# Optimization experiments

Measured on AMD Instinct MI355X. Metric: run time of the kernel, lower is better.

## Reference

```python
import jax, jax.numpy as jnp
import numpy as np

B, ROI, DIN = 1024, 200, 200
ENDS = [41, 70, 91, 110, 130, 137, 158, 200]
STARTS = [0] + ENDS[:-1]
NSUB = len(ENDS)
SEG = np.concatenate([np.full(e - s, i) for i, (s, e) in enumerate(zip(STARTS, ENDS))])  # [ROI]
COUNTS = np.array(ENDS) - np.array(STARTS)
MEAN_MAT = np.zeros((NSUB, ROI), dtype=np.float32)
MEAN_MAT[SEG, np.arange(ROI)] = 1.0 / COUNTS[SEG]
EPS = 1e-5


def _leaky(x):
    return jax.nn.leaky_relu(x, 0.2)


def _bn2d(x, g, b):
    # torch BatchNorm1d (training): biased var over batch dim
    m = x.mean(0)
    v = x.var(0)
    return (x - m) * jax.lax.rsqrt(v + EPS) * g + b


def _bn3d(x, g, b):
    # x: [B, C, L]; stats over (B, L) per channel
    m = x.mean(axis=(0, 2), keepdims=True)
    v = x.var(axis=(0, 2), keepdims=True)
    return (x - m) * jax.lax.rsqrt(v + EPS) * g[None, :, None] + b[None, :, None]


def _block(x, rs_intra, rs_inter, mean_mat, seg):
    # einsum 'ijk,ijp->ijp' == row-sum scaling
    intra = rs_intra * x                                   # [B,R,F]
    sub = jnp.einsum('sr,brf->bsf', mean_mat, x)           # segment means [B,8,F]
    sub = rs_inter * sub                                   # inter row-sum scaling
    prop = sub[:, seg, :]                                  # broadcast back to nodes
    return (intra + prop) * 0.5


def setup_inputs() -> dict:
    key = jax.random.key(0)
    ks = jax.random.split(key, 24)
    s = 0.05
    d = {
        'adjacency_matrix': jax.random.uniform(ks[0], (B, ROI, ROI), jnp.float32),
        'intra_adjacency': jax.random.uniform(ks[1], (B, ROI, ROI), jnp.float32),
        'inter_adjacency': jax.random.uniform(ks[2], (B, NSUB, NSUB), jnp.float32),
        'node_features': jax.random.normal(ks[3], (B, ROI, DIN), jnp.float32),
        'W0': jax.random.normal(ks[4], (DIN, ROI)) * s, 'b0': jnp.zeros((ROI,)),
        'W1': jax.random.normal(ks[5], (ROI, ROI)) * s, 'b1': jnp.zeros((ROI,)),
        'g1': jnp.ones((ROI,)), 'be1': jnp.zeros((ROI,)),
        'W2': jax.random.normal(ks[6], (ROI, ROI)) * s, 'b2': jnp.zeros((ROI,)),
        'g2': jnp.ones((ROI,)), 'be2': jnp.zeros((ROI,)),
        'W3': jax.random.normal(ks[7], (ROI, 64)) * s, 'b3': jnp.zeros((64,)),
        'W4': jax.random.normal(ks[8], (64, 8)) * s, 'b4': jnp.zeros((8,)),
        'g3': jnp.ones((ROI,)), 'be3': jnp.zeros((ROI,)),
        'Wc1': jax.random.normal(ks[9], (8 * ROI, 256)) * s, 'bc1': jnp.zeros((256,)),
        'Wc2': jax.random.normal(ks[10], (256, 32)) * s, 'bc2': jnp.zeros((32,)),
        'Wc3': jax.random.normal(ks[11], (32, 2)) * s, 'bc3': jnp.zeros((2,)),
    }
    return d


def reference(adjacency_matrix, intra_adjacency, inter_adjacency, node_features,
              W0, b0, W1, b1, g1, be1, W2, b2, g2, be2,
              W3, b3, W4, b4, g3, be3, Wc1, bc1, Wc2, bc2, Wc3, bc3):
    mean_mat = jnp.asarray(MEAN_MAT)
    seg = jnp.asarray(SEG)
    rs_intra = intra_adjacency.sum(-1, keepdims=True)   # [B,R,1]
    rs_inter = inter_adjacency.sum(-1, keepdims=True)   # [B,8,1]

    x = _block(node_features, rs_intra, rs_inter, mean_mat, seg)
    x = _leaky(x @ W0 + b0) @ W1 + b1                    # gcn -> [B,R,ROI]
    x = _bn2d(x.reshape(B * ROI, ROI), g1, be1).reshape(B, ROI, ROI)

    x = _block(x, rs_intra, rs_inter, mean_mat, seg)
    x = _leaky(x @ W2 + b2)                              # gcn1
    x = _bn2d(x.reshape(B * ROI, ROI), g2, be2).reshape(B, ROI, ROI)

    x = _block(x, rs_intra, rs_inter, mean_mat, seg)
    x = _leaky(_leaky(x @ W3 + b3) @ W4 + b4)            # gcn2 -> [B,R,8]
    x = _bn3d(x, g3, be3)

    x = x.reshape(B, 8 * ROI)
    x = _leaky(x @ Wc1 + bc1)
    x = _leaky(x @ Wc2 + bc2)
    return x @ Wc3 + bc3
```

## Files before the change

kernel.cpp:

```cpp
#include <hip/hip_runtime.h>
#include <hip/hip_bf16.h>

#define BDIM 1024
#define ROI 200
#define DIN 200
#define NSUB 8
#define NROWS (BDIM * ROI)
#define XELEMS ((size_t)NROWS * 200)
#define PLPAD 32
#define PLSZ (XELEMS + PLPAD)

typedef __attribute__((ext_vector_type(8))) short short8;
typedef __attribute__((ext_vector_type(4))) float f32x4;

__device__ __constant__ float d_invcnt[8] = {
    1.f/41.f, 1.f/29.f, 1.f/21.f, 1.f/19.f, 1.f/20.f, 1.f/7.f, 1.f/21.f, 1.f/42.f};

__device__ inline unsigned short f2bf_rn(float x) {
  unsigned u = __float_as_uint(x);
  return (unsigned short)((u + 0x7FFFu + ((u >> 16) & 1u)) >> 16);
}
__device__ constexpr int seg_of_c(int r) {
  return (r < 41) ? 0 : (r < 70) ? 1 : (r < 91) ? 2 : (r < 110) ? 3
       : (r < 130) ? 4 : (r < 137) ? 5 : (r < 158) ? 6 : 7;
}

__device__ inline void gload_lds16(const unsigned short* src, unsigned short* dst) {
  __builtin_amdgcn_global_load_lds(
      (const __attribute__((address_space(1))) void*)src,
      (__attribute__((address_space(3))) void*)dst, 16, 0, 0);
}

__device__ inline void aburst7(const unsigned short* pA, const unsigned short* pB,
                               short8 (&aA)[7], short8 (&aB)[7]) {
  #pragma unroll
  for (int i = 0; i < 7; ++i) {
    aA[i] = *(const short8*)(pA + i * 32);
    aB[i] = *(const short8*)(pB + i * 32);
  }
}

__global__ __launch_bounds__(256) void rowsum4_k(const float* __restrict__ in,
                                                 float* __restrict__ out) {
  int row = blockIdx.x * 4 + (threadIdx.x >> 6);
  int lane = threadIdx.x & 63;
  const float* p = in + (size_t)row * 200;
  float v = p[lane] + p[lane + 64] + p[lane + 128];
  if (lane < 8) v += p[lane + 192];
  #pragma unroll
  for (int off = 32; off > 0; off >>= 1) v += __shfl_down(v, off);
  if (lane == 0) out[row] = v;
}

__global__ __launch_bounds__(256) void intersum_k(const float* __restrict__ in,
                                                  float* __restrict__ out) {
  int i = blockIdx.x * blockDim.x + threadIdx.x;
  if (i >= BDIM * NSUB) return;
  const float* p = in + (size_t)i * 8;
  float v = 0.f;
  #pragma unroll
  for (int c = 0; c < 8; ++c) v += p[c];
  out[i] = v;
}

template<int INPL, int BN>
__global__ __launch_bounds__(128) void seg_combine_bf_k(
    const float* __restrict__ xf, const unsigned short* __restrict__ xp,
    const float* __restrict__ rsI, const float* __restrict__ rsP,
    const float* __restrict__ ss, unsigned short* __restrict__ yp) {
  int b = blockIdx.x;
  int t = threadIdx.x;
  if (t >= 100) return;
  int c0 = 2 * t;
  size_t base = (size_t)b * 40000 + c0;
  float sc0 = 1.f, sh0 = 0.f, sc1 = 1.f, sh1 = 0.f;
  if (BN) { sc0 = ss[c0]; sh0 = ss[200 + c0]; sc1 = ss[c0 + 1]; sh1 = ss[200 + c0 + 1]; }
  float a0[8] = {0,0,0,0,0,0,0,0};
  float a1[8] = {0,0,0,0,0,0,0,0};
  #pragma unroll
  for (int r = 0; r < 200; ++r) {
    size_t idx = base + (size_t)r * 200;
    float v0, v1;
    if (INPL) {
      unsigned u = *(const unsigned*)(xp + idx);
      v0 = __uint_as_float(u << 16);
      v1 = __uint_as_float(u & 0xFFFF0000u);
    } else {
      float2 fv = *(const float2*)(xf + idx);
      v0 = fv.x; v1 = fv.y;
    }
    int s = seg_of_c(r);
    a0[s] += v0; a1[s] += v1;
  }
  float pr0[8], pr1[8];
  #pragma unroll
  for (int s = 0; s < 8; ++s) {
    float m0 = a0[s] * d_invcnt[s];
    float m1 = a1[s] * d_invcnt[s];
    if (BN) { m0 = m0 * sc0 + sh0; m1 = m1 * sc1 + sh1; }
    float rp = rsP[b * 8 + s];
    pr0[s] = rp * m0; pr1[s] = rp * m1;
  }
  const float* rsIb = rsI + b * 200;
  #pragma unroll
  for (int r = 0; r < 200; ++r) {
    size_t idx = base + (size_t)r * 200;
    float v0, v1;
    if (INPL) {
      unsigned u = *(const unsigned*)(xp + idx);
      v0 = __uint_as_float(u << 16);
      v1 = __uint_as_float(u & 0xFFFF0000u);
    } else {
      float2 fv = *(const float2*)(xf + idx);
      v0 = fv.x; v1 = fv.y;
    }
    if (BN) { v0 = v0 * sc0 + sh0; v1 = v1 * sc1 + sh1; }
    int s = seg_of_c(r);
    float ri = rsIb[r];
    float y0 = 0.5f * (ri * v0 + pr0[s]);
    float y1 = 0.5f * (ri * v1 + pr1[s]);
    unsigned o = (unsigned)f2bf_rn(y0) | ((unsigned)f2bf_rn(y1) << 16);
    *(unsigned*)(yp + idx) = o;
  }
}

__global__ __launch_bounds__(256) void wconv3_k(const float* __restrict__ W, int K, int N,
                                                int NFRAG, int NB, int KSTEPS,
                                                unsigned short* __restrict__ dst) {
  int total = NB * KSTEPS * NFRAG * 64 * 8;
  int idx = blockIdx.x * 256 + threadIdx.x;
  if (idx >= total) return;
  int j = idx & 7;
  int lane = (idx >> 3) & 63;
  int rest = idx >> 9;
  int frag = rest % NFRAG;
  int rest2 = rest / NFRAG;
  int ks = rest2 % KSTEPS;
  int cb = rest2 / KSTEPS;
  int k = ks * 32 + ((lane >> 4) << 3) + j;
  int col = cb * NFRAG * 16 + frag * 16 + (lane & 15);
  float v = (k < K && col < N) ? W[(size_t)k * N + col] : 0.f;
  dst[idx] = f2bf_rn(v);
}

template<int ACT, int STATS>
__global__ __launch_bounds__(512, 1) void gemm_bf3_k(
    const unsigned short* __restrict__ A, const unsigned short* __restrict__ Wf,
    const float* __restrict__ bias, unsigned short* __restrict__ Cp,
    float* __restrict__ stats) {
  constexpr int G = 7 * 7 * 64;
  __shared__ unsigned short wlds[G * 8];
  __shared__ unsigned short abuf[8][2][400 * 8];
  __shared__ float s_sum[112];
  __shared__ float s_sq[112];
  int tid = threadIdx.x;
  int lane = tid & 63;
  int wid = tid >> 6;
  int cb = blockIdx.y;

  const unsigned short* wsrc = Wf + (size_t)cb * G * 8;
  for (int g0 = wid * 64; g0 < G; g0 += 512)
    gload_lds16(wsrc + (size_t)(g0 + lane) * 8, &wlds[(size_t)g0 * 8]);
  if (STATS && tid < 112) { s_sum[tid] = 0.f; s_sq[tid] = 0.f; }

  int gw = blockIdx.x * 8 + wid;
  const int stride = 1024, nt = 12800;
  int row = lane & 15;
  int laneg = lane >> 4;

  auto issue_tile = [&](int t, unsigned short* buf) {
    const unsigned short* src = A + (size_t)t * 3200;
    #pragma unroll
    for (int j = 0; j < 7; ++j) {
      int slot = j * 64 + lane;
      if (slot < 400)
        gload_lds16(src + (size_t)slot * 8, buf + (size_t)j * 512);
    }
  };

  issue_tile(gw, &abuf[wid][0][0]);
  issue_tile(gw + stride, &abuf[wid][1][0]);
  __syncthreads();

  float lsum[7], lsq[7];
  #pragma unroll
  for (int f = 0; f < 7; ++f) { lsum[f] = 0.f; lsq[f] = 0.f; }
  int colbase = cb * 112;

  for (int i = 0; ; ++i) {
    int t = gw + i * stride;
    if (t >= nt) break;
    if (i) {
      asm volatile("s_waitcnt vmcnt(35)" ::: "memory");
      __builtin_amdgcn_sched_barrier(0);
    }
    const unsigned short* ab = &abuf[wid][i & 1][0];
    f32x4 acc[7];
    #pragma unroll
    for (int f = 0; f < 7; ++f) acc[f] = 0.0f;
    #pragma unroll
    for (int ks = 0; ks < 7; ++ks) {
      int cs = ks * 4 + laneg;
      if (cs > 24) cs = 0;
      short8 av = *(const short8*)&ab[(size_t)(row * 25 + cs) * 8];
      const short8* wp = (const short8*)wlds + (size_t)(ks * 7) * 64 + lane;
      #pragma unroll
      for (int f = 0; f < 7; ++f) {
        short8 wv = wp[(size_t)f * 64];
        acc[f] = __builtin_amdgcn_mfma_f32_16x16x32_bf16(av, wv, acc[f], 0, 0, 0);
      }
    }
    asm volatile("s_waitcnt lgkmcnt(0)" ::: "memory");
    __builtin_amdgcn_sched_barrier(0);
    int row0 = t * 16 + laneg * 4;
    #pragma unroll
    for (int f = 0; f < 7; ++f) {
      int col = colbase + f * 16 + row;
      if (col < 200) {
        float b = bias[col];
        #pragma unroll
        for (int r = 0; r < 4; ++r) {
          float v = acc[f][r] + b;
          if (ACT) v = (v >= 0.f) ? v : 0.2f * v;
          Cp[(size_t)(row0 + r) * 200 + col] = f2bf_rn(v);
          if (STATS) { lsum[f] += v; lsq[f] += v * v; }
        }
      }
    }
    __builtin_amdgcn_sched_barrier(0);
    int t2 = t + 2 * stride;
    issue_tile(t2 < nt ? t2 : gw, &abuf[wid][i & 1][0]);
    __builtin_amdgcn_sched_barrier(0);
  }

  if (STATS) {
    #pragma unroll
    for (int f = 0; f < 7; ++f) {
      float s = lsum[f] + __shfl_xor(lsum[f], 16) ;
      s += __shfl_xor(s, 32);
      float q = lsq[f] + __shfl_xor(lsq[f], 16);
      q += __shfl_xor(q, 32);
      if (laneg == 0) {
        atomicAdd(&s_sum[f * 16 + row], s);
        atomicAdd(&s_sq[f * 16 + row], q);
      }
    }
    __syncthreads();
    if (tid < 112) {
      int col = colbase + tid;
      if (col < 200) {
        atomicAdd(&stats[col], s_sum[tid]);
        atomicAdd(&stats[200 + col], s_sq[tid]);
      }
    }
  }
}

__global__ __launch_bounds__(256, 2) void gemm_w34_k(
    const unsigned short* __restrict__ A, const unsigned short* __restrict__ W3f,
    const unsigned short* __restrict__ W4f, const float* __restrict__ b3,
    const float* __restrict__ b4, unsigned short* __restrict__ xcls) {
  __shared__ unsigned short w3lds[7 * 4 * 64 * 8];
  __shared__ unsigned short w4lds[2 * 64 * 8];
  __shared__ unsigned short h3buf[128][72];
  int tid = threadIdx.x;
  int lane = tid & 63;
  int wid = tid >> 6;

  for (int g0 = wid * 64; g0 < 1792; g0 += 256)
    gload_lds16(W3f + (size_t)(g0 + lane) * 8, &w3lds[(size_t)g0 * 8]);
  for (int g0 = wid * 64; g0 < 128; g0 += 256)
    gload_lds16(W4f + (size_t)(g0 + lane) * 8, &w4lds[(size_t)g0 * 8]);

  const unsigned short* baseA = A + (size_t)(lane & 15) * 200 + ((lane >> 4) << 3);
  int r0 = (lane >> 4) * 4;

  short8 aA0[7], aB0[7], aA1[7], aB1[7];
  {
    size_t off = (size_t)(blockIdx.x * 128 + wid * 32) * 200;
    aburst7(baseA + off, baseA + off + 16 * 200, aA0, aB0);
  }
  __builtin_amdgcn_sched_barrier(0);
  __syncthreads();

  #pragma unroll
  for (int t = 0; t < 4; ++t) {
    int rt = blockIdx.x + 400 * t;
    int row0 = rt * 128 + wid * 32;
    if (t < 3) {
      size_t off = (size_t)((rt + 400) * 128 + wid * 32) * 200;
      if (t & 1) aburst7(baseA + off, baseA + off + 16 * 200, aA0, aB0);
      else       aburst7(baseA + off, baseA + off + 16 * 200, aA1, aB1);
      __builtin_amdgcn_sched_barrier(0);
    }
    f32x4 accA[4], accB[4];
    #pragma unroll
    for (int f = 0; f < 4; ++f) { accA[f] = 0.0f; accB[f] = 0.0f; }
    #pragma unroll
    for (int ks = 0; ks < 7; ++ks) {
      const short8* wp = (const short8*)w3lds + (size_t)(ks * 4) * 64 + lane;
      short8 av = (t & 1) ? aA1[ks] : aA0[ks];
      short8 bv = (t & 1) ? aB1[ks] : aB0[ks];
      #pragma unroll
      for (int f = 0; f < 4; ++f) {
        short8 wv = wp[(size_t)f * 64];
        accA[f] = __builtin_amdgcn_mfma_f32_16x16x32_bf16(av, wv, accA[f], 0, 0, 0);
        accB[f] = __builtin_amdgcn_mfma_f32_16x16x32_bf16(bv, wv, accB[f], 0, 0, 0);
      }
    }
    #pragma unroll
    for (int f = 0; f < 4; ++f) {
      int col = f * 16 + (lane & 15);
      float bb = b3[col];
      #pragma unroll
      for (int r = 0; r < 4; ++r) {
        float v = accA[f][r] + bb;
        v = (v >= 0.f) ? v : 0.2f * v;
        h3buf[wid * 32 + r0 + r][col] = f2bf_rn(v);
        v = accB[f][r] + bb;
        v = (v >= 0.f) ? v : 0.2f * v;
        h3buf[wid * 32 + 16 + r0 + r][col] = f2bf_rn(v);
      }
    }
    f32x4 acc2A = 0.0f, acc2B = 0.0f;
    #pragma unroll
    for (int ks = 0; ks < 2; ++ks) {
      short8 a2A = *(const short8*)&h3buf[wid * 32 + (lane & 15)][ks * 32 + ((lane >> 4) << 3)];
      short8 a2B = *(const short8*)&h3buf[wid * 32 + 16 + (lane & 15)][ks * 32 + ((lane >> 4) << 3)];
      short8 wv = *(const short8*)&w4lds[(size_t)(ks * 64 + lane) * 8];
      acc2A = __builtin_amdgcn_mfma_f32_16x16x32_bf16(a2A, wv, acc2A, 0, 0, 0);
      acc2B = __builtin_amdgcn_mfma_f32_16x16x32_bf16(a2B, wv, acc2B, 0, 0, 0);
    }
    int col = lane & 15;
    if (col < 8) {
      float bb = b4[col];
      #pragma unroll
      for (int r = 0; r < 4; ++r) {
        int row = row0 + r0 + r;
        float v = acc2A[r] + bb;
        v = (v >= 0.f) ? v : 0.2f * v;
        xcls[(size_t)(row / 200) * 1600 + (row % 200) * 8 + col] = f2bf_rn(v);
        int row2 = row + 16;
        v = acc2B[r] + bb;
        v = (v >= 0.f) ? v : 0.2f * v;
        xcls[(size_t)(row2 / 200) * 1600 + (row2 % 200) * 8 + col] = f2bf_rn(v);
      }
    }
  }
}

__global__ __launch_bounds__(256) void bn_scale_k(const float* __restrict__ stats,
                                                  const float* __restrict__ g,
                                                  const float* __restrict__ be,
                                                  float invN,
                                                  float* __restrict__ ss) {
  int c = threadIdx.x;
  if (c >= 200) return;
  float m = stats[c] * invN;
  float var = stats[200 + c] * invN - m * m;
  float sc = rsqrtf(var + 1e-5f) * g[c];
  ss[c] = sc;
  ss[200 + c] = be[c] - m * sc;
}

__global__ __launch_bounds__(256) void bn3d_stats_bf_k(const unsigned short* __restrict__ x,
                                                       float* __restrict__ stats) {
  int t = threadIdx.x;
  if (t >= 200) return;
  const unsigned short* p = x + (size_t)blockIdx.x * 16 * 1600 + t * 8;
  float s = 0.f, q = 0.f;
  for (int b = 0; b < 16; ++b) {
    const unsigned* u = (const unsigned*)(p + (size_t)b * 1600);
    #pragma unroll
    for (int i = 0; i < 4; ++i) {
      unsigned w = u[i];
      float v0 = __uint_as_float(w << 16);
      float v1 = __uint_as_float(w & 0xFFFF0000u);
      s += v0 + v1;
      q += v0 * v0 + v1 * v1;
    }
  }
  atomicAdd(&stats[t], s);
  atomicAdd(&stats[200 + t], q);
}

__global__ __launch_bounds__(256) void wcls_conv_k(const float* __restrict__ Wc1,
                                                   const float* __restrict__ ss,
                                                   unsigned short* __restrict__ dst) {
  int idx = blockIdx.x * 256 + threadIdx.x;
  if (idx >= 409600) return;
  int j = idx & 7;
  int lane = (idx >> 3) & 63;
  int rest = idx >> 9;
  int frag = rest & 3;
  int rest2 = rest >> 2;
  int ks = rest2 % 10;
  int slice = rest2 / 10;
  int kc = slice % 5, cb = slice / 5;
  int k = kc * 320 + ks * 32 + ((lane >> 4) << 3) + j;
  int col = cb * 64 + frag * 16 + (lane & 15);
  dst[idx] = f2bf_rn(Wc1[(size_t)k * 256 + col] * ss[k >> 3]);
}

__global__ __launch_bounds__(256) void bias1_init_k(const float* __restrict__ bc1,
                                                    float* __restrict__ bias1p) {
  bias1p[threadIdx.x] = bc1[threadIdx.x];
}
__global__ __launch_bounds__(256) void bias1_acc_k(const float* __restrict__ Wc1,
                                                   const float* __restrict__ ss,
                                                   float* __restrict__ bias1p) {
  int t = threadIdx.x;
  int k0 = blockIdx.x * 100;
  float a = 0.f;
  #pragma unroll 4
  for (int k = k0; k < k0 + 100; ++k)
    a += ss[200 + (k >> 3)] * Wc1[(size_t)k * 256 + t];
  atomicAdd(&bias1p[t], a);
}

__global__ __launch_bounds__(256, 3) void gemm_cls1_k(
    const unsigned short* __restrict__ xcls, const unsigned short* __restrict__ Wf,
    float* __restrict__ h1f) {
  __shared__ unsigned short wlds[10 * 4 * 64 * 8];
  int tid = threadIdx.x;
  int lane = tid & 63;
  int wid = tid >> 6;
  const unsigned short* wsrc = Wf + (size_t)(blockIdx.y * 5 + blockIdx.z) * (10 * 4 * 64) * 8;
  for (int g0 = wid * 64; g0 < 2560; g0 += 256)
    gload_lds16(wsrc + (size_t)(g0 + lane) * 8, &wlds[(size_t)g0 * 8]);

  int row0 = blockIdx.x * 128 + wid * 32;
  int kbase = blockIdx.z * 320;
  const unsigned short* pA = xcls + (size_t)(row0 + (lane & 15)) * 1600 + kbase + ((lane >> 4) << 3);
  const unsigned short* pB = pA + 16 * 1600;
  short8 aA[10], aB[10];
  #pragma unroll
  for (int i = 0; i < 10; ++i) {
    aA[i] = *(const short8*)(pA + i * 32);
    aB[i] = *(const short8*)(pB + i * 32);
  }
  __builtin_amdgcn_sched_barrier(0);
  __syncthreads();

  f32x4 accA[4], accB[4];
  #pragma unroll
  for (int f = 0; f < 4; ++f) { accA[f] = 0.0f; accB[f] = 0.0f; }
  #pragma unroll
  for (int ks = 0; ks < 10; ++ks) {
    const short8* wp = (const short8*)wlds + (size_t)(ks * 4) * 64 + lane;
    #pragma unroll
    for (int f = 0; f < 4; ++f) {
      short8 wv = wp[(size_t)f * 64];
      accA[f] = __builtin_amdgcn_mfma_f32_16x16x32_bf16(aA[ks], wv, accA[f], 0, 0, 0);
      accB[f] = __builtin_amdgcn_mfma_f32_16x16x32_bf16(aB[ks], wv, accB[f], 0, 0, 0);
    }
  }
  int colbase = blockIdx.y * 64;
  int r0 = (lane >> 4) * 4;
  #pragma unroll
  for (int f = 0; f < 4; ++f) {
    int col = colbase + f * 16 + (lane & 15);
    #pragma unroll
    for (int r = 0; r < 4; ++r) {
      atomicAdd(&h1f[(size_t)(row0 + r0 + r) * 256 + col], accA[f][r]);
      atomicAdd(&h1f[(size_t)(row0 + 16 + r0 + r) * 256 + col], accB[f][r]);
    }
  }
}

__global__ __launch_bounds__(256) void classifier2_k(
    const float* __restrict__ h1f, const float* __restrict__ bias1p,
    const float* __restrict__ Wc2, const float* __restrict__ bc2,
    const float* __restrict__ Wc3, const float* __restrict__ bc3,
    float* __restrict__ out) {
  __shared__ float h1s[8][256];
  __shared__ float h2s[8][32];
  int t = threadIdx.x;
  int b0 = blockIdx.x * 8;
  #pragma unroll
  for (int j = 0; j < 8; ++j) {
    float v = h1f[(size_t)(b0 + j) * 256 + t] + bias1p[t];
    h1s[j][t] = (v >= 0.f) ? v : 0.2f * v;
  }
  __syncthreads();
  {
    int j = t >> 5, c = t & 31;
    float a = 0.f;
    #pragma unroll 8
    for (int k = 0; k < 256; ++k) a += h1s[j][k] * Wc2[k * 32 + c];
    float v = a + bc2[c];
    h2s[j][c] = (v >= 0.f) ? v : 0.2f * v;
  }
  __syncthreads();
  if (t < 16) {
    int j = t >> 1, c = t & 1;
    float a = 0.f;
    #pragma unroll
    for (int k = 0; k < 32; ++k) a += h2s[j][k] * Wc3[k * 2 + c];
    out[(size_t)(b0 + j) * 2 + c] = a + bc3[c];
  }
}

extern "C" void kernel_launch(void* const* d_in, const int* in_sizes, int n_in,
                              void* d_out, int out_size, void* d_ws, size_t ws_size,
                              hipStream_t stream) {
  const float* intra = (const float*)d_in[1];
  const float* inter = (const float*)d_in[2];
  const float* nodef = (const float*)d_in[3];
  const float* W0 = (const float*)d_in[4];
  const float* b0 = (const float*)d_in[5];
  const float* W1 = (const float*)d_in[6];
  const float* b1 = (const float*)d_in[7];
  const float* g1 = (const float*)d_in[8];
  const float* be1 = (const float*)d_in[9];
  const float* W2 = (const float*)d_in[10];
  const float* b2 = (const float*)d_in[11];
  const float* g2 = (const float*)d_in[12];
  const float* be2 = (const float*)d_in[13];
  const float* W3 = (const float*)d_in[14];
  const float* b3 = (const float*)d_in[15];
  const float* W4 = (const float*)d_in[16];
  const float* b4 = (const float*)d_in[17];
  const float* g3 = (const float*)d_in[18];
  const float* be3 = (const float*)d_in[19];
  const float* Wc1 = (const float*)d_in[20];
  const float* bc1 = (const float*)d_in[21];
  const float* Wc2 = (const float*)d_in[22];
  const float* bc2 = (const float*)d_in[23];
  const float* Wc3 = (const float*)d_in[24];
  const float* bc3 = (const float*)d_in[25];
  float* out = (float*)d_out;

  unsigned short* P0 = (unsigned short*)d_ws;
  unsigned short* P1 = P0 + PLSZ;
  float* fbase = (float*)(P1 + PLSZ);
  float* rsI  = fbase;
  float* rsP  = rsI + NROWS;
  float* stats = rsP + BDIM * 8;
  float* ssbuf = stats + 512;
  float* h1f  = ssbuf + 512;
  float* bias1p = h1f + (size_t)BDIM * 256;
  unsigned short* wt = (unsigned short*)(bias1p + 512);
  const size_t W200SZ = 2 * 7 * 7 * 64 * 8;
  const size_t W3SZ   = 1 * 7 * 4 * 64 * 8;
  const size_t W4SZ   = 1 * 2 * 1 * 64 * 8;
  unsigned short* w0f = wt;
  unsigned short* w1f = w0f + W200SZ;
  unsigned short* w2f = w1f + W200SZ;
  unsigned short* w3f = w2f + W200SZ;
  unsigned short* w4f = w3f + W3SZ;
  unsigned short* wc1f = w4f + W4SZ;
  unsigned short* xcls = P0;

  hipMemsetAsync(P0 + XELEMS, 0, PLPAD * 2, stream);
  hipMemsetAsync(P1 + XELEMS, 0, PLPAD * 2, stream);

  wconv3_k<<<(int)((W200SZ + 255) / 256), 256, 0, stream>>>(W0, 200, 200, 7, 2, 7, w0f);
  wconv3_k<<<(int)((W200SZ + 255) / 256), 256, 0, stream>>>(W1, 200, 200, 7, 2, 7, w1f);
  wconv3_k<<<(int)((W200SZ + 255) / 256), 256, 0, stream>>>(W2, 200, 200, 7, 2, 7, w2f);
  wconv3_k<<<(int)((W3SZ + 255) / 256), 256, 0, stream>>>(W3, 200, 64, 4, 1, 7, w3f);
  wconv3_k<<<(int)((W4SZ + 255) / 256), 256, 0, stream>>>(W4, 64, 8, 1, 1, 2, w4f);

  rowsum4_k<<<NROWS / 4, 256, 0, stream>>>(intra, rsI);
  intersum_k<<<(BDIM * 8 + 255) / 256, 256, 0, stream>>>(inter, rsP);

  seg_combine_bf_k<0, 0><<<BDIM, 128, 0, stream>>>(
      nodef, nullptr, rsI, rsP, nullptr, P0);

  gemm_bf3_k<1, 0><<<dim3(128, 2), 512, 0, stream>>>(P0, w0f, b0, P1, nullptr);
  hipMemsetAsync(stats, 0, 400 * sizeof(float), stream);
  gemm_bf3_k<0, 1><<<dim3(128, 2), 512, 0, stream>>>(P1, w1f, b1, P0, stats);
  bn_scale_k<<<1, 256, 0, stream>>>(stats, g1, be1, 1.f / (float)NROWS, ssbuf);

  seg_combine_bf_k<1, 1><<<BDIM, 128, 0, stream>>>(
      nullptr, P0, rsI, rsP, ssbuf, P1);

  hipMemsetAsync(stats, 0, 400 * sizeof(float), stream);
  gemm_bf3_k<1, 1><<<dim3(128, 2), 512, 0, stream>>>(P1, w2f, b2, P0, stats);
  bn_scale_k<<<1, 256, 0, stream>>>(stats, g2, be2, 1.f / (float)NROWS, ssbuf);

  seg_combine_bf_k<1, 1><<<BDIM, 128, 0, stream>>>(
      nullptr, P0, rsI, rsP, ssbuf, P1);

  gemm_w34_k<<<400, 256, 0, stream>>>(P1, w3f, w4f, b3, b4, xcls);

  hipMemsetAsync(stats, 0, 400 * sizeof(float), stream);
  bn3d_stats_bf_k<<<64, 256, 0, stream>>>(xcls, stats);
  bn_scale_k<<<1, 256, 0, stream>>>(stats, g3, be3, 1.f / 8192.f, ssbuf);

  wcls_conv_k<<<1600, 256, 0, stream>>>(Wc1, ssbuf, wc1f);
  bias1_init_k<<<1, 256, 0, stream>>>(bc1, bias1p);
  bias1_acc_k<<<16, 256, 0, stream>>>(Wc1, ssbuf, bias1p);

  hipMemsetAsync(h1f, 0, (size_t)BDIM * 256 * sizeof(float), stream);
  gemm_cls1_k<<<dim3(8, 4, 5), 256, 0, stream>>>(xcls, wc1f, h1f);
  classifier2_k<<<BDIM / 8, 256, 0, stream>>>(h1f, bias1p, Wc2, bc2, Wc3, bc3, out);
}
```

Before: 429.4 us.

## Rewrite W3/W4 GEMM as persistent kernel with async LDS double-buffering

```diff
diff --git a/kernel.cpp b/kernel.cpp
--- a/kernel.cpp
+++ b/kernel.cpp
@@ -29,15 +29,6 @@
   __builtin_amdgcn_global_load_lds(
       (const __attribute__((address_space(1))) void*)src,
       (__attribute__((address_space(3))) void*)dst, 16, 0, 0);
-}
-
-__device__ inline void aburst7(const unsigned short* pA, const unsigned short* pB,
-                               short8 (&aA)[7], short8 (&aB)[7]) {
-  #pragma unroll
-  for (int i = 0; i < 7; ++i) {
-    aA[i] = *(const short8*)(pA + i * 32);
-    aB[i] = *(const short8*)(pB + i * 32);
-  }
 }
 
 __global__ __launch_bounds__(256) void rowsum4_k(const float* __restrict__ in,
@@ -191,7 +182,7 @@
     int t = gw + i * stride;
     if (t >= nt) break;
     if (i) {
-      asm volatile("s_waitcnt vmcnt(35)" ::: "memory");
+      asm volatile("s_waitcnt vmcnt(24)" ::: "memory");
       __builtin_amdgcn_sched_barrier(0);
     }
     const unsigned short* ab = &abuf[wid][i & 1][0];
@@ -236,7 +227,7 @@
   if (STATS) {
     #pragma unroll
     for (int f = 0; f < 7; ++f) {
-      float s = lsum[f] + __shfl_xor(lsum[f], 16) ;
+      float s = lsum[f] + __shfl_xor(lsum[f], 16);
       s += __shfl_xor(s, 32);
       float q = lsq[f] + __shfl_xor(lsq[f], 16);
       q += __shfl_xor(q, 32);
@@ -256,96 +247,102 @@
   }
 }
 
-__global__ __launch_bounds__(256, 2) void gemm_w34_k(
+__global__ __launch_bounds__(512, 1) void gemm_w34s_k(
     const unsigned short* __restrict__ A, const unsigned short* __restrict__ W3f,
     const unsigned short* __restrict__ W4f, const float* __restrict__ b3,
     const float* __restrict__ b4, unsigned short* __restrict__ xcls) {
-  __shared__ unsigned short w3lds[7 * 4 * 64 * 8];
-  __shared__ unsigned short w4lds[2 * 64 * 8];
-  __shared__ unsigned short h3buf[128][72];
+  __shared__ unsigned short w3lds[1792 * 8];
+  __shared__ unsigned short w4lds[128 * 8];
+  __shared__ unsigned short abuf[8][2][400 * 8];
+  __shared__ unsigned short h3buf[8][16][72];
   int tid = threadIdx.x;
   int lane = tid & 63;
   int wid = tid >> 6;
 
-  for (int g0 = wid * 64; g0 < 1792; g0 += 256)
+  for (int g0 = wid * 64; g0 < 1792; g0 += 512)
     gload_lds16(W3f + (size_t)(g0 + lane) * 8, &w3lds[(size_t)g0 * 8]);
-  for (int g0 = wid * 64; g0 < 128; g0 += 256)
-    gload_lds16(W4f + (size_t)(g0 + lane) * 8, &w4lds[(size_t)g0 * 8]);
-
-  const unsigned short* baseA = A + (size_t)(lane & 15) * 200 + ((lane >> 4) << 3);
-  int r0 = (lane >> 4) * 4;
-
-  short8 aA0[7], aB0[7], aA1[7], aB1[7];
-  {
-    size_t off = (size_t)(blockIdx.x * 128 + wid * 32) * 200;
-    aburst7(baseA + off, baseA + off + 16 * 200, aA0, aB0);
-  }
-  __builtin_amdgcn_sched_barrier(0);
+  if (wid == 0)
+    for (int g0 = 0; g0 < 128; g0 += 64)
+      gload_lds16(W4f + (size_t)(g0 + lane) * 8, &w4lds[(size_t)g0 * 8]);
+
+  int gw = blockIdx.x * 8 + wid;
+  const int stride = 1024, nt = 12800;
+  int row = lane & 15;
+  int laneg = lane >> 4;
+
+  auto issue_tile = [&](int t, unsigned short* buf) {
+    const unsigned short* src = A + (size_t)t * 3200;
+    #pragma unroll
+    for (int j = 0; j < 7; ++j) {
+      int slot = j * 64 + lane;
+      if (slot < 400)
+        gload_lds16(src + (size_t)slot * 8, buf + (size_t)j * 512);
+    }
+  };
+
+  issue_tile(gw, &abuf[wid][0][0]);
+  issue_tile(gw + stride, &abuf[wid][1][0]);
   __syncthreads();
 
-  #pragma unroll
-  for (int t = 0; t < 4; ++t) {
-    int rt = blockIdx.x + 400 * t;
-    int row0 = rt * 128 + wid * 32;
-    if (t < 3) {
-      size_t off = (size_t)((rt + 400) * 128 + wid * 32) * 200;
-      if (t & 1) aburst7(baseA + off, baseA + off + 16 * 200, aA0, aB0);
-      else       aburst7(baseA + off, baseA + off + 16 * 200, aA1, aB1);
+  for (int i = 0; ; ++i) {
+    int t = gw + i * stride;
+    if (t >= nt) break;
+    if (i) {
+      asm volatile("s_waitcnt vmcnt(8)" ::: "memory");
       __builtin_amdgcn_sched_barrier(0);
     }
-    f32x4 accA[4], accB[4];
-    #pragma unroll
-    for (int f = 0; f < 4; ++f) { accA[f] = 0.0f; accB[f] = 0.0f; }
+    const unsigned short* ab = &abuf[wid][i & 1][0];
+    f32x4 acc[4];
+    #pragma unroll
+    for (int f = 0; f < 4; ++f) acc[f] = 0.0f;
     #pragma unroll
     for (int ks = 0; ks < 7; ++ks) {
+      int cs = ks * 4 + laneg;
+      if (cs > 24) cs = 0;
+      short8 av = *(const short8*)&ab[(size_t)(row * 25 + cs) * 8];
       const short8* wp = (const short8*)w3lds + (size_t)(ks * 4) * 64 + lane;
-      short8 av = (t & 1) ? aA1[ks] : aA0[ks];
-      short8 bv = (t & 1) ? aB1[ks] : aB0[ks];
       #pragma unroll
       for (int f = 0; f < 4; ++f) {
         short8 wv = wp[(size_t)f * 64];
-        accA[f] = __builtin_amdgcn_mfma_f32_16x16x32_bf16(av, wv, accA[f], 0, 0, 0);
-        accB[f] = __builtin_amdgcn_mfma_f32_16x16x32_bf16(bv, wv, accB[f], 0, 0, 0);
-      }
-    }
+        acc[f] = __builtin_amdgcn_mfma_f32_16x16x32_bf16(av, wv, acc[f], 0, 0, 0);
+      }
+    }
+    int r0 = laneg * 4;
     #pragma unroll
     for (int f = 0; f < 4; ++f) {
-      int col = f * 16 + (lane & 15);
+      int col = f * 16 + row;
       float bb = b3[col];
       #pragma unroll
       for (int r = 0; r < 4; ++r) {
-        float v = accA[f][r] + bb;
+        float v = acc[f][r] + bb;
         v = (v >= 0.f) ? v : 0.2f * v;
-        h3buf[wid * 32 + r0 + r][col] = f2bf_rn(v);
-        v = accB[f][r] + bb;
-        v = (v >= 0.f) ? v : 0.2f * v;
-        h3buf[wid * 32 + 16 + r0 + r][col] = f2bf_rn(v);
-      }
-    }
-    f32x4 acc2A = 0.0f, acc2B = 0.0f;
+        h3buf[wid][r0 + r][col] = f2bf_rn(v);
+      }
+    }
+    f32x4 acc2 = 0.0f;
     #pragma unroll
     for (int ks = 0; ks < 2; ++ks) {
-      short8 a2A = *(const short8*)&h3buf[wid * 32 + (lane & 15)][ks * 32 + ((lane >> 4) << 3)];
-      short8 a2B = *(const short8*)&h3buf[wid * 32 + 16 + (lane & 15)][ks * 32 + ((lane >> 4) << 3)];
+      short8 a2 = *(const short8*)&h3buf[wid][row][ks * 32 + laneg * 8];
       short8 wv = *(const short8*)&w4lds[(size_t)(ks * 64 + lane) * 8];
-      acc2A = __builtin_amdgcn_mfma_f32_16x16x32_bf16(a2A, wv, acc2A, 0, 0, 0);
-      acc2B = __builtin_amdgcn_mfma_f32_16x16x32_bf16(a2B, wv, acc2B, 0, 0, 0);
-    }
+      acc2 = __builtin_amdgcn_mfma_f32_16x16x32_bf16(a2, wv, acc2, 0, 0, 0);
+    }
+    asm volatile("s_waitcnt lgkmcnt(0)" ::: "memory");
+    __builtin_amdgcn_sched_barrier(0);
     int col = lane & 15;
     if (col < 8) {
       float bb = b4[col];
       #pragma unroll
       for (int r = 0; r < 4; ++r) {
-        int row = row0 + r0 + r;
-        float v = acc2A[r] + bb;
+        int rr = t * 16 + r0 + r;
+        float v = acc2[r] + bb;
         v = (v >= 0.f) ? v : 0.2f * v;
-        xcls[(size_t)(row / 200) * 1600 + (row % 200) * 8 + col] = f2bf_rn(v);
-        int row2 = row + 16;
-        v = acc2B[r] + bb;
-        v = (v >= 0.f) ? v : 0.2f * v;
-        xcls[(size_t)(row2 / 200) * 1600 + (row2 % 200) * 8 + col] = f2bf_rn(v);
-      }
-    }
+        xcls[(size_t)(rr / 200) * 1600 + (rr % 200) * 8 + col] = f2bf_rn(v);
+      }
+    }
+    __builtin_amdgcn_sched_barrier(0);
+    int t2 = t + 2 * stride;
+    issue_tile(t2 < nt ? t2 : gw, &abuf[wid][i & 1][0]);
+    __builtin_amdgcn_sched_barrier(0);
   }
 }
 
@@ -582,7 +579,7 @@
   seg_combine_bf_k<1, 1><<<BDIM, 128, 0, stream>>>(
       nullptr, P0, rsI, rsP, ssbuf, P1);
 
-  gemm_w34_k<<<400, 256, 0, stream>>>(P1, w3f, w4f, b3, b4, xcls);
+  gemm_w34s_k<<<128, 512, 0, stream>>>(P1, w3f, w4f, b3, b4, xcls);
 
   hipMemsetAsync(stats, 0, 400 * sizeof(float), stream);
   bn3d_stats_bf_k<<<64, 256, 0, stream>>>(xcls, stats);
```

After: 431.8 us. About the same (+0.6%).
